# Kernel tuning notes

Measured on AMD Instinct MI355X. Metric: run time of the kernel, lower is better.

Reference implementation:

```python
import jax, jax.numpy as jnp
import numpy as np
import math

HIDDEN = 3072
N_HEADS = 32
N_KV_HEADS = 32
HEAD_DIM = HIDDEN // N_HEADS  # 96
ROPE_THETA = 10000.0
ORIG_MAX_POS = 4096
MAX_POS = 131072
SHORT_FACTOR = np.ones(HEAD_DIM // 2, dtype=np.float32)  # length 48 rope scaling factors
SCALING_FACTOR = math.sqrt(1.0 + math.log(MAX_POS / ORIG_MAX_POS) / math.log(ORIG_MAX_POS))


def setup_inputs() -> dict:
    key = jax.random.key(0)
    k1, k2, k3 = jax.random.split(key, 3)
    B, L = 2, 2048
    x = jax.random.normal(k1, (B, L, HIDDEN), dtype=jnp.float32)
    op_size = N_HEADS * HEAD_DIM + 2 * (N_KV_HEADS * HEAD_DIM)
    Wqkv = jax.random.normal(k2, (op_size, HIDDEN), dtype=jnp.float32) * (HIDDEN ** -0.5)
    Wo = jax.random.normal(k3, (HIDDEN, HIDDEN), dtype=jnp.float32) * (HIDDEN ** -0.5)
    return {"x": x, "Wqkv": Wqkv, "Wo": Wo}


def _rope_cos_sin(L):
    # SuScaled RoPE; L <= ORIG_MAX_POS so short_factor is used
    ext = jnp.asarray(SHORT_FACTOR)
    inv_freq_shape = jnp.arange(0, HEAD_DIM, 2, dtype=jnp.float32) / HEAD_DIM
    inv_freq = 1.0 / (ext * (ROPE_THETA ** inv_freq_shape))  # [Hd/2]
    pos = jnp.arange(L, dtype=jnp.float32)
    freqs = pos[:, None] * inv_freq[None, :]  # [L, Hd/2]
    emb = jnp.concatenate([freqs, freqs], axis=-1)  # [L, Hd]
    cos = jnp.cos(emb) * SCALING_FACTOR
    sin = jnp.sin(emb) * SCALING_FACTOR
    return cos[None, None, :, :], sin[None, None, :, :]  # [1,1,L,Hd]


def _rotate_half(t):
    mid = t.shape[-1] // 2
    return jnp.concatenate([-t[..., mid:], t[..., :mid]], axis=-1)


def reference(x, Wqkv, Wo):
    B, L, D = x.shape
    qkv = jnp.einsum('bld,od->blo', x, Wqkv)  # [B,L,op_size]
    qpos = N_HEADS * HEAD_DIM
    kpos = qpos + N_KV_HEADS * HEAD_DIM
    q = qkv[..., :qpos].reshape(B, L, N_HEADS, HEAD_DIM).transpose(0, 2, 1, 3)
    k = qkv[..., qpos:kpos].reshape(B, L, N_KV_HEADS, HEAD_DIM).transpose(0, 2, 1, 3)
    v = qkv[..., kpos:].reshape(B, L, N_KV_HEADS, HEAD_DIM).transpose(0, 2, 1, 3)

    cos, sin = _rope_cos_sin(L)
    q = q * cos + _rotate_half(q) * sin
    k = k * cos + _rotate_half(k) * sin

    scale = HEAD_DIM ** -0.5
    scores = jnp.einsum('bhqd,bhkd->bhqk', q * scale, k)  # [B,H,L,L]
    causal = jnp.triu(jnp.full((L, L), -jnp.inf, dtype=scores.dtype), k=1)
    scores = scores + causal[None, None, :, :]
    probs = jax.nn.softmax(scores, axis=-1)
    out = jnp.einsum('bhqk,bhkd->bhqd', probs, v)  # [B,H,L,Hd]
    out = out.transpose(0, 2, 1, 3).reshape(B, L, N_HEADS * HEAD_DIM)
    return jnp.einsum('blo,do->bld', out, Wo)  # o_proj
```

## Files before the change

### kernel.cpp

```cpp
#include <hip/hip_runtime.h>
#include <cstdint>

typedef short s16x8 __attribute__((ext_vector_type(8)));
typedef float f32x4 __attribute__((ext_vector_type(4)));
typedef unsigned short u16;

#define DEV static __device__ __forceinline__

DEV float bf2f(u16 b) {
  union { unsigned u; float f; } v; v.u = ((unsigned)b) << 16; return v.f;
}
DEV u16 f2bf(float f) {
  union { float f; unsigned u; } v; v.f = f;
  unsigned r = 0x7fffu + ((v.u >> 16) & 1u);
  return (u16)((v.u + r) >> 16);
}

typedef __attribute__((address_space(3))) void lds_void_t;
typedef const __attribute__((address_space(1))) void glob_void_t;

DEV void async_copy16(const void* g, void* l) {
  __builtin_amdgcn_global_load_lds(
      (glob_void_t*)(uintptr_t)g,
      (lds_void_t*)(uint32_t)(uintptr_t)l,
      16, 0, 0);
}

__global__ void cvt_f32_bf16(const float* __restrict__ in, u16* __restrict__ out, int n4) {
  int i = blockIdx.x * 256 + threadIdx.x;
  if (i < n4) {
    const float4 v = reinterpret_cast<const float4*>(in)[i];
    ushort4 o;
    o.x = f2bf(v.x); o.y = f2bf(v.y); o.z = f2bf(v.z); o.w = f2bf(v.w);
    reinterpret_cast<ushort4*>(out)[i] = o;
  }
}

template <bool OUT_BF16>
__global__ __launch_bounds__(256, 2)
void gemm_nt(const u16* __restrict__ A, const u16* __restrict__ B,
             void* __restrict__ C, int M, int N, int K) {
  __shared__ u16 As[128 * 32];
  __shared__ u16 Bs[128 * 32];
  const int tid  = threadIdx.x;
  const int lane = tid & 63;
  const int wave = tid >> 6;
  const int wr = wave >> 1, wc = wave & 1;
  const int l15 = lane & 15, quad = lane >> 4;
  const int bm = blockIdx.x, bn = blockIdx.y;

  const int srow   = lane >> 2;
  const int schunk = (lane & 3) ^ ((srow >> 1) & 3);
  const int fsw    = (l15 >> 1) & 3;

  f32x4 acc[4][4];
  const f32x4 zero4 = {0.f, 0.f, 0.f, 0.f};
#pragma unroll
  for (int i = 0; i < 4; ++i)
#pragma unroll
    for (int j = 0; j < 4; ++j) acc[i][j] = zero4;

  const size_t Abase = (size_t)(bm * 128) * K;
  const size_t Bbase = (size_t)(bn * 128) * K;

  for (int kt = 0; kt < K; kt += 32) {
#pragma unroll
    for (int c = 0; c < 2; ++c) {
      const int grp = wave * 2 + c;
      const int row = grp * 16 + srow;
      const u16* gA = A + Abase + (size_t)row * K + kt + schunk * 8;
      const u16* gB = B + Bbase + (size_t)row * K + kt + schunk * 8;
      async_copy16(gA, As + grp * 512 + lane * 8);
      async_copy16(gB, Bs + grp * 512 + lane * 8);
    }
    __syncthreads();

    s16x8 af[4], bf[4];
#pragma unroll
    for (int mi = 0; mi < 4; ++mi) {
      const int row = wr * 64 + mi * 16 + l15;
      af[mi] = *(const s16x8*)(As + row * 32 + (quad ^ fsw) * 8);
    }
#pragma unroll
    for (int ni = 0; ni < 4; ++ni) {
      const int row = wc * 64 + ni * 16 + l15;
      bf[ni] = *(const s16x8*)(Bs + row * 32 + (quad ^ fsw) * 8);
    }
#pragma unroll
    for (int mi = 0; mi < 4; ++mi)
#pragma unroll
      for (int ni = 0; ni < 4; ++ni)
        acc[mi][ni] = __builtin_amdgcn_mfma_f32_16x16x32_bf16(af[mi], bf[ni], acc[mi][ni], 0, 0, 0);
    __syncthreads();
  }

#pragma unroll
  for (int mi = 0; mi < 4; ++mi) {
#pragma unroll
    for (int ni = 0; ni < 4; ++ni) {
      const int gm0 = bm * 128 + wr * 64 + mi * 16 + quad * 4;
      const int gn  = bn * 128 + wc * 64 + ni * 16 + l15;
#pragma unroll
      for (int r = 0; r < 4; ++r) {
        const size_t idx = (size_t)(gm0 + r) * N + gn;
        if (OUT_BF16) ((u16*)C)[idx] = f2bf(acc[mi][ni][r]);
        else          ((float*)C)[idx] = acc[mi][ni][r];
      }
    }
  }
}

__global__ void rope_split(const u16* __restrict__ qkv, u16* __restrict__ Q,
                           u16* __restrict__ Kb, u16* __restrict__ Vt) {
  const int tok = blockIdx.x;
  const int b = tok >> 11, l = tok & 2047;
  const float pos = (float)l;
  const float SF = 1.1902380714238083f;
  const float QSCALE = 0.10206207261596575f;
  const size_t base = (size_t)tok * 9216;
  for (int i = threadIdx.x; i < 768; i += 256) {
    const int g = i * 4;
    const int h = g / 96, d0 = g - h * 96;
    const ushort4 qv4 = *(const ushort4*)(qkv + base + g);
    const ushort4 kv4 = *(const ushort4*)(qkv + base + 3072 + g);
    const ushort4 vv4 = *(const ushort4*)(qkv + base + 6144 + g);
    const int dp0    = (d0 < 48) ? d0 + 48 : d0 - 48;
    const float sgn  = (d0 < 48) ? -1.0f : 1.0f;
    const ushort4 qp4 = *(const ushort4*)(qkv + base + h * 96 + dp0);
    const ushort4 kp4 = *(const ushort4*)(qkv + base + 3072 + h * 96 + dp0);
    const int fi0 = (d0 < 48) ? d0 : d0 - 48;
    const int bh = b * 32 + h;
    ushort4 qo, ko;
    const u16* qvp = (const u16*)&qv4; const u16* kvp = (const u16*)&kv4;
    const u16* qpp = (const u16*)&qp4; const u16* kpp = (const u16*)&kp4;
    const u16* vvp = (const u16*)&vv4;
    u16* qop = (u16*)&qo; u16* kop = (u16*)&ko;
#pragma unroll
    for (int e = 0; e < 4; ++e) {
      const float inv = exp2f(-13.287712379549449f * ((float)(fi0 + e) * (1.0f / 48.0f)));
      const float ang = pos * inv;
      float s, c;
      sincosf(ang, &s, &c);
      c *= SF; s *= SF;
      const float qout = bf2f(qvp[e]) * c + bf2f(qpp[e]) * sgn * s;
      const float kout = bf2f(kvp[e]) * c + bf2f(kpp[e]) * sgn * s;
      qop[e] = f2bf(qout * QSCALE);
      kop[e] = f2bf(kout);
      Vt[((size_t)bh * 96 + d0 + e) * 2048 + l] = vvp[e];
    }
    *(ushort4*)(Q  + ((size_t)bh * 2048 + l) * 96 + d0) = qo;
    *(ushort4*)(Kb + ((size_t)bh * 2048 + l) * 96 + d0) = ko;
  }
}

__global__ __launch_bounds__(256, 3)
void attn(const u16* __restrict__ Q, const u16* __restrict__ Kb,
          const u16* __restrict__ Vt, u16* __restrict__ ctx) {
  const int qb = 31 - blockIdx.x;
  const int bh = blockIdx.y;
  const int tid = threadIdx.x, lane = tid & 63, wave = tid >> 6;
  const int l15 = lane & 15, quad = lane >> 4;

  __shared__ alignas(16) u16 Kl[2][64 * 104];
  __shared__ alignas(16) u16 Vl[2][96 * 64];

  const size_t hbase = (size_t)bh * 2048 * 96;
  const int q0 = qb * 64 + wave * 16;

  s16x8 aq[3];
#pragma unroll
  for (int c = 0; c < 3; ++c)
    aq[c] = *(const s16x8*)(Q + hbase + (size_t)(q0 + l15) * 96 + c * 32 + quad * 8);

  float m_ = -1e30f, l_ = 0.f;
  f32x4 o[6];
  const f32x4 zero4 = {0.f, 0.f, 0.f, 0.f};
#pragma unroll
  for (int d = 0; d < 6; ++d) o[d] = zero4;

  auto stage = [&](int buf, int kb) {
    const int k0 = kb * 64;
    for (int j = wave; j < 13; j += 4) {
      const int id = j * 64 + lane;
      const int k  = id / 13;
      const int cc = id - k * 13;
      const u16* src = Kb + hbase + (size_t)(k0 + k) * 96 + (cc < 12 ? cc * 8 : 0);
      async_copy16(src, &Kl[buf][j * 512 + lane * 8]);
    }
    for (int j = wave; j < 12; j += 4) {
      const int id = j * 64 + lane;
      const int d  = id >> 3;
      const int lc = (id & 7) ^ (d & 7);
      const u16* src = Vt + ((size_t)bh * 96 + d) * 2048 + k0 + lc * 8;
      async_copy16(src, &Vl[buf][j * 512 + lane * 8]);
    }
  };

  stage(0, 0);
  __syncthreads();
  int cur = 0;

  const int addrA = (l15 + (quad & 1) * 32) * 4;
  const int addrB = addrA + 64;
  const bool hb = (quad >= 2);

  for (int kb = 0; kb <= qb; ++kb) {
    if (kb < qb) stage(cur ^ 1, kb + 1);
    const int k0 = kb * 64;
    const bool last = (kb == qb);
    const int nsub   = last ? (wave + 1) : 4;
    const int nchunk = last ? ((wave >> 1) + 1) : 2;

    f32x4 s[4];
#pragma unroll
    for (int sub = 0; sub < 4; ++sub) {
      if (sub < nsub) {
        const u16* kr = &Kl[cur][(sub * 16 + l15) * 104 + quad * 8];
        const s16x8 b0 = *(const s16x8*)(kr);
        const s16x8 b1 = *(const s16x8*)(kr + 32);
        const s16x8 b2 = *(const s16x8*)(kr + 64);
        f32x4 t = __builtin_amdgcn_mfma_f32_16x16x32_bf16(b0, aq[0], zero4, 0, 0, 0);
        t = __builtin_amdgcn_mfma_f32_16x16x32_bf16(b1, aq[1], t, 0, 0, 0);
        t = __builtin_amdgcn_mfma_f32_16x16x32_bf16(b2, aq[2], t, 0, 0, 0);
        s[sub] = t;
      } else {
        s[sub] = (f32x4){-1e30f, -1e30f, -1e30f, -1e30f};
      }
    }

    if (last) {
      const int q = q0 + l15;
#pragma unroll
      for (int sub = 0; sub < 4; ++sub)
#pragma unroll
        for (int r = 0; r < 4; ++r) {
          const int k = k0 + sub * 16 + quad * 4 + r;
          if (k > q) s[sub][r] = -1e30f;
        }
    }

    float mx = s[0][0];
#pragma unroll
    for (int sub = 0; sub < 4; ++sub)
#pragma unroll
      for (int r = 0; r < 4; ++r) mx = fmaxf(mx, s[sub][r]);
    mx = fmaxf(mx, __shfl_xor(mx, 16));
    mx = fmaxf(mx, __shfl_xor(mx, 32));
    const float mn = fmaxf(m_, mx);
    const float al = __expf(m_ - mn);
    m_ = mn;
#pragma unroll
    for (int sub = 0; sub < 4; ++sub)
#pragma unroll
      for (int r = 0; r < 4; ++r) s[sub][r] = __expf(s[sub][r] - mn);
    float rs = (((s[0][0] + s[0][1]) + (s[0][2] + s[0][3])) +
                ((s[1][0] + s[1][1]) + (s[1][2] + s[1][3]))) +
               (((s[2][0] + s[2][1]) + (s[2][2] + s[2][3])) +
                ((s[3][0] + s[3][1]) + (s[3][2] + s[3][3])));
    rs += __shfl_xor(rs, 16);
    rs += __shfl_xor(rs, 32);
    l_ = l_ * al + rs;

    float alr[4];
#pragma unroll
    for (int r = 0; r < 4; ++r)
      alr[r] = __int_as_float(__builtin_amdgcn_ds_bpermute((quad * 4 + r) * 4,
                                                           __float_as_int(al)));
#pragma unroll
    for (int d = 0; d < 6; ++d)
#pragma unroll
      for (int r = 0; r < 4; ++r) o[d][r] *= alr[r];

    unsigned pk[4][2];
#pragma unroll
    for (int sub = 0; sub < 4; ++sub) {
      asm("v_cvt_pk_bf16_f32 %0, %1, %2" : "=v"(pk[sub][0]) : "v"(s[sub][0]), "v"(s[sub][1]));
      asm("v_cvt_pk_bf16_f32 %0, %1, %2" : "=v"(pk[sub][1]) : "v"(s[sub][2]), "v"(s[sub][3]));
    }

#pragma unroll
    for (int c = 0; c < 2; ++c) {
      if (c < nchunk) {
        const int a00 = __builtin_amdgcn_ds_bpermute(addrA, (int)pk[c * 2][0]);
        const int a01 = __builtin_amdgcn_ds_bpermute(addrA, (int)pk[c * 2][1]);
        const int a10 = __builtin_amdgcn_ds_bpermute(addrA, (int)pk[c * 2 + 1][0]);
        const int a11 = __builtin_amdgcn_ds_bpermute(addrA, (int)pk[c * 2 + 1][1]);
        const int b00 = __builtin_amdgcn_ds_bpermute(addrB, (int)pk[c * 2][0]);
        const int b01 = __builtin_amdgcn_ds_bpermute(addrB, (int)pk[c * 2][1]);
        const int b10 = __builtin_amdgcn_ds_bpermute(addrB, (int)pk[c * 2 + 1][0]);
        const int b11 = __builtin_amdgcn_ds_bpermute(addrB, (int)pk[c * 2 + 1][1]);
        union { s16x8 v; int u[4]; } ap;
        ap.u[0] = hb ? a10 : a00;
        ap.u[1] = hb ? a11 : a01;
        ap.u[2] = hb ? b10 : b00;
        ap.u[3] = hb ? b11 : b01;
#pragma unroll
        for (int dblk = 0; dblk < 6; ++dblk) {
          const int d = dblk * 16 + l15;
          const s16x8 bv = *(const s16x8*)(&Vl[cur][d * 64 + (((c * 4 + quad) ^ (d & 7)) * 8)]);
          o[dblk] = __builtin_amdgcn_mfma_f32_16x16x32_bf16(ap.v, bv, o[dblk], 0, 0, 0);
        }
      }
    }

    __syncthreads();
    cur ^= 1;
  }

  const int b = bh >> 5, h = bh & 31;
  float invl[4];
#pragma unroll
  for (int r = 0; r < 4; ++r) {
    const int v = __builtin_amdgcn_ds_bpermute((quad * 4 + r) * 4, __float_as_int(l_));
    invl[r] = 1.0f / __int_as_float(v);
  }
#pragma unroll
  for (int d = 0; d < 6; ++d)
#pragma unroll
    for (int r = 0; r < 4; ++r) {
      const int row = q0 + quad * 4 + r;
      ctx[((size_t)(b * 2048 + row)) * 3072 + h * 96 + d * 16 + l15] = f2bf(o[d][r] * invl[r]);
    }
}

extern "C" void kernel_launch(void* const* d_in, const int* in_sizes, int n_in,
                              void* d_out, int out_size, void* d_ws, size_t ws_size,
                              hipStream_t stream) {
  const float* x    = (const float*)d_in[0];
  const float* Wqkv = (const float*)d_in[1];
  const float* Wo   = (const float*)d_in[2];
  float* out = (float*)d_out;

  char* ws = (char*)d_ws;
  u16* wq_b  = (u16*)(ws);
  u16* wo_b  = (u16*)(ws + 56623104);
  u16* x_b   = (u16*)(ws + 75497472);
  u16* qkv_b = (u16*)(ws + 100663296);
  u16* K_b   = (u16*)(ws + 176160768);
  u16* Vt_b  = (u16*)(ws + 201326592);
  u16* Q_b   = x_b;
  u16* ctx_b = qkv_b;

  cvt_f32_bf16<<<27648, 256, 0, stream>>>(Wqkv, wq_b, 28311552 / 4);
  cvt_f32_bf16<<<9216,  256, 0, stream>>>(Wo,   wo_b,  9437184 / 4);
  cvt_f32_bf16<<<12288, 256, 0, stream>>>(x,    x_b,  12582912 / 4);

  gemm_nt<true><<<dim3(32, 72), 256, 0, stream>>>(x_b, wq_b, (void*)qkv_b, 4096, 9216, 3072);

  rope_split<<<4096, 256, 0, stream>>>(qkv_b, Q_b, K_b, Vt_b);

  attn<<<dim3(32, 64), 256, 0, stream>>>(Q_b, K_b, Vt_b, ctx_b);

  gemm_nt<false><<<dim3(32, 24), 256, 0, stream>>>(ctx_b, wo_b, (void*)out, 4096, 3072, 3072);
}
```

Measured before the change: 908.0 us.

## Replace GEMM with 256x256 tiled, double-buffered kernel with XCD-aware block swizzle

Replaces the 128x128, K=32, single-buffer GEMM with a 256x256 tile, K=64 step kernel using 512 threads and double-buffered LDS that prefetches the next K tile while computing the current one. It also remaps the 1D block index across the 8 XCDs for L2 locality, and uses setprio and barriers around the MFMA bursts. The aim is more data reuse per load and hiding global-to-LDS latency. In exchange it uses 128KB of LDS per block, so launch_bounds(512,2) likely cannot be met and occupancy drops. The o_proj GEMM also gets only 192 blocks, which may underfill the GPU.

```diff
diff --git a/kernel.cpp b/kernel.cpp
--- a/kernel.cpp
+++ b/kernel.cpp
@@ -37,69 +37,100 @@
 }
 
 template <bool OUT_BF16>
-__global__ __launch_bounds__(256, 2)
-void gemm_nt(const u16* __restrict__ A, const u16* __restrict__ B,
-             void* __restrict__ C, int M, int N, int K) {
-  __shared__ u16 As[128 * 32];
-  __shared__ u16 Bs[128 * 32];
+__global__ __launch_bounds__(512, 2)
+void gemm_nt256(const u16* __restrict__ A, const u16* __restrict__ B,
+                void* __restrict__ C, int M, int N, int K) {
+  __shared__ u16 As[2][256 * 64];
+  __shared__ u16 Bs[2][256 * 64];
   const int tid  = threadIdx.x;
   const int lane = tid & 63;
   const int wave = tid >> 6;
-  const int wr = wave >> 1, wc = wave & 1;
+  const int wm = wave >> 2, wn = wave & 3;
   const int l15 = lane & 15, quad = lane >> 4;
-  const int bm = blockIdx.x, bn = blockIdx.y;
-
-  const int srow   = lane >> 2;
-  const int schunk = (lane & 3) ^ ((srow >> 1) & 3);
-  const int fsw    = (l15 >> 1) & 3;
-
-  f32x4 acc[4][4];
+
+  const int nwg = gridDim.x;
+  const int cpx = nwg >> 3;
+  const int swz = (blockIdx.x & 7) * cpx + (blockIdx.x >> 3);
+  const int mb  = M >> 8;
+  const int bm  = swz % mb, bn = swz / mb;
+
+  f32x4 acc[8][4];
   const f32x4 zero4 = {0.f, 0.f, 0.f, 0.f};
 #pragma unroll
-  for (int i = 0; i < 4; ++i)
-#pragma unroll
-    for (int j = 0; j < 4; ++j) acc[i][j] = zero4;
-
-  const size_t Abase = (size_t)(bm * 128) * K;
-  const size_t Bbase = (size_t)(bn * 128) * K;
-
-  for (int kt = 0; kt < K; kt += 32) {
-#pragma unroll
-    for (int c = 0; c < 2; ++c) {
-      const int grp = wave * 2 + c;
-      const int row = grp * 16 + srow;
-      const u16* gA = A + Abase + (size_t)row * K + kt + schunk * 8;
-      const u16* gB = B + Bbase + (size_t)row * K + kt + schunk * 8;
-      async_copy16(gA, As + grp * 512 + lane * 8);
-      async_copy16(gB, Bs + grp * 512 + lane * 8);
+  for (int mi = 0; mi < 8; ++mi)
+#pragma unroll
+    for (int ni = 0; ni < 4; ++ni) acc[mi][ni] = zero4;
+
+  const size_t Abase = (size_t)(bm * 256) * K;
+  const size_t Bbase = (size_t)(bn * 256) * K;
+
+  auto stage = [&](int buf, int kt) {
+#pragma unroll
+    for (int j = 0; j < 4; ++j) {
+      const int id  = j * 512 + tid;
+      const int row = id >> 3;
+      const int sc  = ((id & 7) ^ (row & 7)) * 8;
+      async_copy16(A + Abase + (size_t)row * K + kt + sc, &As[buf][id * 8]);
+    }
+#pragma unroll
+    for (int j = 0; j < 4; ++j) {
+      const int id  = j * 512 + tid;
+      const int row = id >> 3;
+      const int sc  = ((id & 7) ^ (row & 7)) * 8;
+      async_copy16(B + Bbase + (size_t)row * K + kt + sc, &Bs[buf][id * 8]);
+    }
+  };
+
+  stage(0, 0);
+  __syncthreads();
+  int cur = 0;
+  const int NT = K >> 6;
+
+  for (int t = 0; t < NT; ++t) {
+    if (t + 1 < NT) stage(cur ^ 1, (t + 1) << 6);
+
+    s16x8 bfr[2][4];
+#pragma unroll
+    for (int ks = 0; ks < 2; ++ks)
+#pragma unroll
+      for (int ni = 0; ni < 4; ++ni) {
+        const int row = wn * 64 + ni * 16 + l15;
+        bfr[ks][ni] = *(const s16x8*)(&Bs[cur][row * 64 + ((ks * 4 + quad) ^ (row & 7)) * 8]);
+      }
+
+#pragma unroll
+    for (int qd = 0; qd < 4; ++qd) {
+      s16x8 afr[2][2];
+#pragma unroll
+      for (int ks = 0; ks < 2; ++ks)
+#pragma unroll
+        for (int mm = 0; mm < 2; ++mm) {
+          const int row = wm * 128 + (qd * 2 + mm) * 16 + l15;
+          afr[ks][mm] = *(const s16x8*)(&As[cur][row * 64 + ((ks * 4 + quad) ^ (row & 7)) * 8]);
+        }
+      __builtin_amdgcn_s_barrier();
+      __builtin_amdgcn_sched_barrier(0);
+      __builtin_amdgcn_s_setprio(1);
+#pragma unroll
+      for (int ks = 0; ks < 2; ++ks)
+#pragma unroll
+        for (int mm = 0; mm < 2; ++mm)
+#pragma unroll
+          for (int ni = 0; ni < 4; ++ni)
+            acc[qd * 2 + mm][ni] = __builtin_amdgcn_mfma_f32_16x16x32_bf16(
+                afr[ks][mm], bfr[ks][ni], acc[qd * 2 + mm][ni], 0, 0, 0);
+      __builtin_amdgcn_s_setprio(0);
     }
     __syncthreads();
-
-    s16x8 af[4], bf[4];
-#pragma unroll
-    for (int mi = 0; mi < 4; ++mi) {
-      const int row = wr * 64 + mi * 16 + l15;
-      af[mi] = *(const s16x8*)(As + row * 32 + (quad ^ fsw) * 8);
-    }
+    cur ^= 1;
+  }
+
+#pragma unroll
+  for (int mi = 0; mi < 8; ++mi) {
 #pragma unroll
     for (int ni = 0; ni < 4; ++ni) {
-      const int row = wc * 64 + ni * 16 + l15;
-      bf[ni] = *(const s16x8*)(Bs + row * 32 + (quad ^ fsw) * 8);
-    }
-#pragma unroll
-    for (int mi = 0; mi < 4; ++mi)
-#pragma unroll
-      for (int ni = 0; ni < 4; ++ni)
-        acc[mi][ni] = __builtin_amdgcn_mfma_f32_16x16x32_bf16(af[mi], bf[ni], acc[mi][ni], 0, 0, 0);
-    __syncthreads();
-  }
-
-#pragma unroll
-  for (int mi = 0; mi < 4; ++mi) {
-#pragma unroll
-    for (int ni = 0; ni < 4; ++ni) {
-      const int gm0 = bm * 128 + wr * 64 + mi * 16 + quad * 4;
-      const int gn  = bn * 128 + wc * 64 + ni * 16 + l15;
+      const int gm0 = bm * 256 + wm * 128 + mi * 16 + quad * 4;
+      const int gn  = bn * 256 + wn * 64 + ni * 16 + l15;
 #pragma unroll
       for (int r = 0; r < 4; ++r) {
         const size_t idx = (size_t)(gm0 + r) * N + gn;
@@ -345,11 +376,11 @@
   cvt_f32_bf16<<<9216,  256, 0, stream>>>(Wo,   wo_b,  9437184 / 4);
   cvt_f32_bf16<<<12288, 256, 0, stream>>>(x,    x_b,  12582912 / 4);
 
-  gemm_nt<true><<<dim3(32, 72), 256, 0, stream>>>(x_b, wq_b, (void*)qkv_b, 4096, 9216, 3072);
+  gemm_nt256<true><<<576, 512, 0, stream>>>(x_b, wq_b, (void*)qkv_b, 4096, 9216, 3072);
 
   rope_split<<<4096, 256, 0, stream>>>(qkv_b, Q_b, K_b, Vt_b);
 
   attn<<<dim3(32, 64), 256, 0, stream>>>(Q_b, K_b, Vt_b, ctx_b);
 
-  gemm_nt<false><<<dim3(32, 24), 256, 0, stream>>>(ctx_b, wo_b, (void*)out, 4096, 3072, 3072);
-}
+  gemm_nt256<false><<<192, 512, 0, stream>>>(ctx_b, wo_b, (void*)out, 4096, 3072, 3072);
+}
```

After: 878.3 us. 1.03x faster.
